# Kernel tuning notes

Measured on AMD Instinct MI355X. Metric: run time of the kernel, lower is better.

Reference implementation:

```python
import jax, jax.numpy as jnp
import numpy as np

N = 100000   # nodes
E = 1600000  # edges (before self-loops)
F_IN = 128
H = 64
G = 512      # graphs in batch


def _add_self_loops(edge_index, n):
    loop = jnp.arange(n, dtype=edge_index.dtype)
    src = jnp.concatenate([edge_index[0], loop])
    dst = jnp.concatenate([edge_index[1], loop])
    return src, dst


def _gcn_norm(src, dst, n):
    # PyG GCNConv: deg over targets with self-loops, norm = d^-1/2[src]*d^-1/2[dst]
    deg = jax.ops.segment_sum(jnp.ones_like(dst, dtype=jnp.float32), dst, num_segments=n)
    dinv = jnp.where(deg > 0, jax.lax.rsqrt(deg), 0.0)
    return dinv[src] * dinv[dst]


def _gcn_conv(x, src, dst, norm, W, b):
    xw = x @ W                                # [N, H]
    msg = xw[src] * norm[:, None]             # [E+N, H] gather + scale
    out = jax.ops.segment_sum(msg, dst, num_segments=x.shape[0])
    return out + b


def setup_inputs() -> dict:
    key = jax.random.key(0)
    ks = jax.random.split(key, 9)
    x = jax.random.normal(ks[0], (N, F_IN), dtype=jnp.float32)
    edge_index = jax.random.randint(ks[1], (2, E), 0, N, dtype=jnp.int32)
    batch = jnp.sort(jax.random.randint(ks[2], (N,), 0, G, dtype=jnp.int32))
    s1 = 1.0 / np.sqrt(F_IN)
    s2 = 1.0 / np.sqrt(H)
    W1 = jax.random.uniform(ks[3], (F_IN, H), jnp.float32, -s1, s1)
    b1 = jnp.zeros((H,), jnp.float32)
    W2 = jax.random.uniform(ks[4], (H, H), jnp.float32, -s2, s2)
    b2 = jnp.zeros((H,), jnp.float32)
    Wl = jax.random.uniform(ks[5], (H, 1), jnp.float32, -s2, s2)
    bl = jnp.zeros((1,), jnp.float32)
    return {"x": x, "edge_index": edge_index, "batch": batch,
            "W1": W1, "b1": b1, "W2": W2, "b2": b2, "Wl": Wl, "bl": bl}


def reference(x, edge_index, batch, W1, b1, W2, b2, Wl, bl):
    n = x.shape[0]
    src, dst = _add_self_loops(edge_index, n)
    norm = _gcn_norm(src, dst, n)
    h = jax.nn.relu(_gcn_conv(x, src, dst, norm, W1, b1))
    h = jax.nn.relu(_gcn_conv(h, src, dst, norm, W2, b2))
    # global mean pool over graphs
    sums = jax.ops.segment_sum(h, batch, num_segments=G)          # [G, H]
    cnt = jax.ops.segment_sum(jnp.ones((n,), jnp.float32), batch, num_segments=G)
    pooled = sums / jnp.maximum(cnt, 1.0)[:, None]
    return jax.nn.sigmoid(pooled @ Wl + bl)                        # [G, 1]
```

## Files before the change

### kernel.cpp

```cpp
#include <hip/hip_runtime.h>
#include <hip/hip_bf16.h>
#include <cmath>

#define F_IN 128
#define HDIM 64
#define NPB 128
#define NB1 512
#define CAP 2560

typedef __attribute__((ext_vector_type(8))) short bf16x8;
typedef __attribute__((ext_vector_type(4))) float f32x4;
typedef __attribute__((ext_vector_type(2))) float f32x2;

__device__ __forceinline__ float bf2f(unsigned short u) {
    union { unsigned int i; float f; } v; v.i = ((unsigned int)u) << 16; return v.f;
}
__device__ __forceinline__ unsigned short f2bf(float f) {
    __hip_bfloat16 h = __float2bfloat16(f);
    union { __hip_bfloat16 h; unsigned short u; } c; c.h = h; return c.u;
}
__device__ __forceinline__ unsigned char f2fp8(float f) {
    int p = __builtin_amdgcn_cvt_pk_fp8_f32(f, f, 0, false);
    return (unsigned char)(p & 0xff);
}
__device__ __forceinline__ void fp8x8_acc(uint2 v, float* a) {
    f32x2 f;
    f = __builtin_amdgcn_cvt_pk_f32_fp8(v.x, false); a[0] += f.x; a[1] += f.y;
    f = __builtin_amdgcn_cvt_pk_f32_fp8(v.x, true);  a[2] += f.x; a[3] += f.y;
    f = __builtin_amdgcn_cvt_pk_f32_fp8(v.y, false); a[4] += f.x; a[5] += f.y;
    f = __builtin_amdgcn_cvt_pk_f32_fp8(v.y, true);  a[6] += f.x; a[7] += f.y;
}


__launch_bounds__(256)
__global__ void p0_count(const int* __restrict__ dst, int* __restrict__ blk_cnt,
                         int E, int nbuk, int chunk,
                         const float* __restrict__ W1, const float* __restrict__ W2,
                         unsigned short* __restrict__ w1t, unsigned short* __restrict__ w2t) {
    int tid = threadIdx.x;
    if (blockIdx.x >= NB1) {
        int t = (blockIdx.x - NB1) * 256 + tid;
        if (t < F_IN * 64) {
            int c = t & 63, k = t >> 6;
            w1t[c * F_IN + k] = f2bf(W1[t]);
        } else if (t < F_IN * 64 + HDIM * 64) {
            int u = t - F_IN * 64;
            int c = u & 63, k = u >> 6;
            w2t[c * HDIM + k] = f2bf(W2[u]);
        }
        return;
    }
    __shared__ int hist[1024];
    for (int i = tid; i < nbuk; i += 256) hist[i] = 0;
    __syncthreads();
    int lo = blockIdx.x * chunk, hi = min(E, lo + chunk);
    for (int e = lo + tid; e < hi; e += 256)
        atomicAdd(&hist[dst[e] >> 7], 1);
    __syncthreads();
    for (int i = tid; i < nbuk; i += 256)
        blk_cnt[(size_t)i * NB1 + blockIdx.x] = hist[i];
}


__launch_bounds__(256)
__global__ void p_scan_blocks(int* __restrict__ blk_cnt, int* __restrict__ bucket_cnt,
                              int nbuk, const int* __restrict__ batch,
                              int* __restrict__ gstart, int n, int G) {
    int tid = threadIdx.x;
    if (blockIdx.x >= nbuk) {
        int g = (blockIdx.x - nbuk) * 256 + tid;
        if (g > G) return;
        int lo = 0, hi = n;
        while (lo < hi) {
            int mid = (lo + hi) >> 1;
            if (batch[mid] < g) lo = mid + 1; else hi = mid;
        }
        gstart[g] = lo;
        return;
    }
    __shared__ int sd[256];
    int b = blockIdx.x;
    int2* row = (int2*)(blk_cnt + (size_t)b * NB1);
    int2 v = row[tid];
    int s0 = v.x, s1 = s0 + v.y;
    sd[tid] = s1;
    __syncthreads();
    for (int off = 1; off < 256; off <<= 1) {
        int a = (tid >= off) ? sd[tid - off] : 0;
        __syncthreads();
        sd[tid] += a;
        __syncthreads();
    }
    int base = sd[tid] - s1;
    row[tid] = make_int2(base, base + s0);
    if (tid == 255) bucket_cnt[b] = sd[255];
}


__launch_bounds__(256)
__global__ void p1_place(const int* __restrict__ src, const int* __restrict__ dst,
                         const int* __restrict__ blk_cnt, int* __restrict__ pairs,
                         int E, int nbuk, int chunk) {
    __shared__ int cur[1024];
    int tid = threadIdx.x;
    for (int i = tid; i < nbuk; i += 256)
        cur[i] = i * CAP + blk_cnt[(size_t)i * NB1 + blockIdx.x];
    __syncthreads();
    int lo = blockIdx.x * chunk, hi = min(E, lo + chunk);
    for (int e = lo + tid; e < hi; e += 256) {
        int d = dst[e];
        int pos = atomicAdd(&cur[d >> 7], 1);
        pairs[pos] = (src[e] << 7) | (d & 127);
    }
}


__launch_bounds__(256)
__global__ void p2_csr(const int* __restrict__ pairs, const int* __restrict__ bucket_cnt,
                       float* __restrict__ dinv, int* __restrict__ col,
                       int4* __restrict__ slot_hdr, int n) {
    __shared__ int dl[128];
    __shared__ int sc[128];
    __shared__ int cur[128];
    __shared__ int h64[64];
    __shared__ int s64[64];
    int b = blockIdx.x, tid = threadIdx.x;
    int nlo = b << 7;
    int eb = b * CAP;
    int ee = eb + bucket_cnt[b];
    if (tid < 128) dl[tid] = 0;
    if (tid < 64) h64[tid] = 0;
    __syncthreads();
    for (int e = eb + tid; e < ee; e += 256)
        atomicAdd(&dl[pairs[e] & 127], 1);
    __syncthreads();
    int d0 = 0, excl = 0;
    if (tid < 128) { d0 = dl[tid]; sc[tid] = d0; }
    __syncthreads();
    for (int off = 1; off < 128; off <<= 1) {
        int a = (tid >= off && tid < 128) ? sc[tid - off] : 0;
        __syncthreads();
        if (tid < 128) sc[tid] += a;
        __syncthreads();
    }
    if (tid < 128) {
        excl = sc[tid] - d0;
        int node = nlo + tid;
        float dv = rsqrtf((float)(d0 + 1));
        if (node < n) dinv[node] = dv;
        cur[tid] = eb + excl;
        atomicAdd(&h64[min(d0, 63)], 1);
    }
    __syncthreads();
    if (tid == 0) { int run = 0; for (int i = 0; i < 64; ++i) { s64[i] = run; run += h64[i]; } }
    __syncthreads();
    if (tid < 64) h64[tid] = 0;
    __syncthreads();
    if (tid < 128) {
        int node = nlo + tid;
        int bin = min(d0, 63);
        int pos = s64[bin] + atomicAdd(&h64[bin], 1);
        int4 hdr;
        hdr.x = (node < n) ? node : 0x7fffffff;
        hdr.y = eb + excl;
        hdr.z = d0;
        hdr.w = __float_as_int(rsqrtf((float)(d0 + 1)));
        slot_hdr[nlo + pos] = hdr;
    }
    __syncthreads();
    for (int e = eb + tid; e < ee; e += 256) {
        unsigned int v = (unsigned int)pairs[e];
        int pos = atomicAdd(&cur[v & 127], 1);
        col[pos] = (int)(v >> 7);
    }
}


template <int K>
__launch_bounds__(256)
__global__ void matmul_mfma(const float* __restrict__ X, const unsigned short* __restrict__ Wt,
                            const float* __restrict__ dinv, unsigned char* __restrict__ out,
                            int n) {
    constexpr int KS  = K / 32;
    constexpr int LDX = K + 8;
    __shared__ unsigned short Xs[64 * LDX];
    __shared__ unsigned short Ws[64 * LDX];
    int tid = threadIdx.x;
    int rowbase = blockIdx.x * 64;
    for (int i = tid; i < 64 * (K / 8); i += 256) {
        int r = i / (K / 8), ch = i % (K / 8);
        *(bf16x8*)(Ws + r * LDX + ch * 8) = ((const bf16x8*)Wt)[i];
    }
    {
        const float4* X4 = (const float4*)X;
        for (int i = tid; i < 64 * (K / 4); i += 256) {
            int r = i / (K / 4), k4 = i % (K / 4);
            ushort4 u = { 0, 0, 0, 0 };
            int gr = rowbase + r;
            if (gr < n) {
                float4 v = X4[(size_t)gr * (K / 4) + k4];
                u.x = f2bf(v.x); u.y = f2bf(v.y); u.z = f2bf(v.z); u.w = f2bf(v.w);
            }
            *(ushort4*)(Xs + r * LDX + k4 * 4) = u;
        }
    }
    __syncthreads();
    int wave = tid >> 6, lane = tid & 63;
    int q = lane >> 4, nn = lane & 15;
    f32x4 acc[4] = {{0,0,0,0},{0,0,0,0},{0,0,0,0},{0,0,0,0}};
    int mrow = wave * 16 + nn;
#pragma unroll
    for (int s = 0; s < KS; ++s) {
        bf16x8 af = *(const bf16x8*)(Xs + mrow * LDX + s * 32 + q * 8);
#pragma unroll
        for (int c = 0; c < 4; ++c) {
            bf16x8 bf = *(const bf16x8*)(Ws + (c * 16 + nn) * LDX + s * 32 + q * 8);
            acc[c] = __builtin_amdgcn_mfma_f32_16x16x32_bf16(af, bf, acc[c], 0, 0, 0);
        }
    }
#pragma unroll
    for (int r = 0; r < 4; ++r) {
        int row = rowbase + wave * 16 + q * 4 + r;
        if (row >= n) continue;
        float dv = dinv[row];
#pragma unroll
        for (int c = 0; c < 4; ++c)
            out[(size_t)row * HDIM + c * 16 + nn] = f2fp8(acc[c][r] * dv);
    }
}


__launch_bounds__(256)
__global__ void gather1_mm2(const int4* __restrict__ slot_hdr, const int* __restrict__ col,
                            const uint2* __restrict__ xws, const float* __restrict__ bias,
                            const unsigned short* __restrict__ w2t,
                            unsigned char* __restrict__ out8, int nslots, int n) {
    __shared__ unsigned short Hs[32 * 72];
    __shared__ unsigned short Ws[64 * 72];
    __shared__ int   snode[32];
    __shared__ float sdinv[32];

    int tid = threadIdx.x;
    int ls = tid >> 3;
    int L  = tid & 7;
    int slot = blockIdx.x * 32 + ls;

    for (int i = tid; i < 64 * 8; i += 256) {
        int r = i >> 3, ch = i & 7;
        *(bf16x8*)(Ws + r * 72 + ch * 8) = ((const bf16x8*)w2t)[i];
    }

    int node = 0x7fffffff;
    float dv = 0.0f;
    float a[8] = {0, 0, 0, 0, 0, 0, 0, 0};
    if (slot < nslots) {
        int4 hdr = slot_hdr[slot];
        node = hdr.x;
        if (node < n) {
            int s = hdr.y, end = s + hdr.z;
            dv = __int_as_float(hdr.w);
            fp8x8_acc(xws[(size_t)node * 8 + L], a);
            int e = s;
            for (; e + 8 <= end; e += 8) {
                uint2 v0 = xws[(size_t)col[e + 0] * 8 + L];
                uint2 v1 = xws[(size_t)col[e + 1] * 8 + L];
                uint2 v2 = xws[(size_t)col[e + 2] * 8 + L];
                uint2 v3 = xws[(size_t)col[e + 3] * 8 + L];
                uint2 v4 = xws[(size_t)col[e + 4] * 8 + L];
                uint2 v5 = xws[(size_t)col[e + 5] * 8 + L];
                uint2 v6 = xws[(size_t)col[e + 6] * 8 + L];
                uint2 v7 = xws[(size_t)col[e + 7] * 8 + L];
                fp8x8_acc(v0, a); fp8x8_acc(v1, a); fp8x8_acc(v2, a); fp8x8_acc(v3, a);
                fp8x8_acc(v4, a); fp8x8_acc(v5, a); fp8x8_acc(v6, a); fp8x8_acc(v7, a);
            }
            for (; e < end; ++e)
                fp8x8_acc(xws[(size_t)col[e] * 8 + L], a);
        }
    }
    if (L == 0) { snode[ls] = node; sdinv[ls] = dv; }
    {
        int f0 = L * 8;
        bf16x8 o;
        if (node < n) {
#pragma unroll
            for (int j = 0; j < 8; ++j)
                o[j] = (short)f2bf(fmaxf(fmaf(a[j], dv, bias[f0 + j]), 0.0f));
        } else {
            short z[8] = {0,0,0,0,0,0,0,0};
            o = *(bf16x8*)z;
        }
        *(bf16x8*)(Hs + ls * 72 + L * 8) = o;
    }
    __syncthreads();

    int wave = tid >> 6, lane = tid & 63;
    int q = lane >> 4, nn = lane & 15;
    int mt  = wave & 1;
    int nt0 = (wave >> 1) * 2;
    f32x4 acc[2] = {{0,0,0,0},{0,0,0,0}};
#pragma unroll
    for (int s = 0; s < 2; ++s) {
        bf16x8 af = *(const bf16x8*)(Hs + (mt * 16 + nn) * 72 + s * 32 + q * 8);
#pragma unroll
        for (int t = 0; t < 2; ++t) {
            bf16x8 bf = *(const bf16x8*)(Ws + ((nt0 + t) * 16 + nn) * 72 + s * 32 + q * 8);
            acc[t] = __builtin_amdgcn_mfma_f32_16x16x32_bf16(af, bf, acc[t], 0, 0, 0);
        }
    }
#pragma unroll
    for (int r = 0; r < 4; ++r) {
        int lslot = mt * 16 + q * 4 + r;
        int nd = snode[lslot];
        if (nd >= n) continue;
        float dvr = sdinv[lslot];
#pragma unroll
        for (int t = 0; t < 2; ++t)
            out8[(size_t)nd * HDIM + (nt0 + t) * 16 + nn] = f2fp8(acc[t][r] * dvr);
    }
}


__launch_bounds__(256)
__global__ void csr_gather8_fp8(const int4* __restrict__ slot_hdr, const int* __restrict__ col,
                                const uint2* __restrict__ xws, const float* __restrict__ bias,
                                bf16x8* __restrict__ outb, int nslots, int n) {
    int t = blockIdx.x * 256 + threadIdx.x;
    int slot = t >> 3;
    if (slot >= nslots) return;
    int L = t & 7;
    int4 hdr = slot_hdr[slot];
    int node = hdr.x;
    if (node >= n) return;
    int s = hdr.y, end = s + hdr.z;
    float dv = __int_as_float(hdr.w);

    float a[8] = {0, 0, 0, 0, 0, 0, 0, 0};
    fp8x8_acc(xws[(size_t)node * 8 + L], a);
    int e = s;
    for (; e + 8 <= end; e += 8) {
        uint2 v0 = xws[(size_t)col[e + 0] * 8 + L];
        uint2 v1 = xws[(size_t)col[e + 1] * 8 + L];
        uint2 v2 = xws[(size_t)col[e + 2] * 8 + L];
        uint2 v3 = xws[(size_t)col[e + 3] * 8 + L];
        uint2 v4 = xws[(size_t)col[e + 4] * 8 + L];
        uint2 v5 = xws[(size_t)col[e + 5] * 8 + L];
        uint2 v6 = xws[(size_t)col[e + 6] * 8 + L];
        uint2 v7 = xws[(size_t)col[e + 7] * 8 + L];
        fp8x8_acc(v0, a); fp8x8_acc(v1, a); fp8x8_acc(v2, a); fp8x8_acc(v3, a);
        fp8x8_acc(v4, a); fp8x8_acc(v5, a); fp8x8_acc(v6, a); fp8x8_acc(v7, a);
    }
    for (; e < end; ++e)
        fp8x8_acc(xws[(size_t)col[e] * 8 + L], a);

    int f0 = L * 8;
    bf16x8 o;
#pragma unroll
    for (int j = 0; j < 8; ++j)
        o[j] = (short)f2bf(fmaxf(fmaf(a[j], dv, bias[f0 + j]), 0.0f));
    outb[(size_t)node * 8 + L] = o;
}


__launch_bounds__(256)
__global__ void pool_head(const unsigned short* __restrict__ h, const int* __restrict__ gstart,
                          const float* __restrict__ Wl, const float* __restrict__ bl,
                          float* __restrict__ out, int G) {
    int g = blockIdx.x;
    int s = gstart[g], e = gstart[g + 1];
    int f  = threadIdx.x & 63;
    int rg = threadIdx.x >> 6;
    float acc = 0.0f;
    for (int i = s + rg; i < e; i += 4)
        acc += bf2f(h[(size_t)i * HDIM + f]);
    __shared__ float red[4][HDIM];
    red[rg][f] = acc;
    __syncthreads();
    if (rg == 0) {
        float v = (red[0][f] + red[1][f]) + (red[2][f] + red[3][f]);
        float c = fmaxf((float)(e - s), 1.0f);
        v = v * Wl[f] * (1.0f / c);
#pragma unroll
        for (int off = 32; off; off >>= 1) v += __shfl_down(v, off, 64);
        if (f == 0) out[g] = 1.0f / (1.0f + expf(-(v + bl[0])));
    }
}


extern "C" void kernel_launch(void* const* d_in, const int* in_sizes, int n_in,
                              void* d_out, int out_size, void* d_ws, size_t ws_size,
                              hipStream_t stream) {
    const float* x   = (const float*)d_in[0];
    const int* ei    = (const int*)d_in[1];
    const int* batch = (const int*)d_in[2];
    const float* W1  = (const float*)d_in[3];
    const float* b1  = (const float*)d_in[4];
    const float* W2  = (const float*)d_in[5];
    const float* b2  = (const float*)d_in[6];
    const float* Wl  = (const float*)d_in[7];
    const float* bl  = (const float*)d_in[8];
    float* out = (float*)d_out;

    const int n = in_sizes[0] / F_IN;
    const int E = in_sizes[1] / 2;
    const int G = out_size;

    const int* srcp = ei;
    const int* dstp = ei + E;

    int nbuk = (n + NPB - 1) / NPB;
    int nslots = nbuk * NPB;

    char* wsb = (char*)d_ws;
    auto alloc = [&](size_t bytes) { char* p = wsb; wsb += (bytes + 255) & ~(size_t)255; return p; };
    float* dinv       = (float*)alloc((size_t)n * 4);
    int4*  slot_hdr   = (int4*)alloc((size_t)nslots * 16);
    int*   bucket_cnt = (int*)alloc(1024 * 4);
    int*   blk_cnt    = (int*)alloc((size_t)nbuk * NB1 * 4);
    int*   pairs      = (int*)alloc((size_t)nbuk * CAP * 4);
    int*   colx       = (int*)alloc((size_t)nbuk * CAP * 4);
    unsigned short* w1t  = (unsigned short*)alloc((size_t)F_IN * HDIM * 2);
    unsigned short* w2t  = (unsigned short*)alloc((size_t)HDIM * HDIM * 2);
    unsigned char*  xws8 = (unsigned char*)alloc((size_t)n * HDIM);
    unsigned char*  xws8b= (unsigned char*)alloc((size_t)n * HDIM);
    unsigned short* xh2  = (unsigned short*)alloc((size_t)n * HDIM * 2);
    int*   gstart     = (int*)alloc(((size_t)G + 1) * 4);

    const int TB = 256;
    int gMM  = (n + 63) / 64;
    int chunk = (E + NB1 - 1) / NB1;
    int gG8  = (nslots * 8 + TB - 1) / TB;
    int gS   = (nslots + 31) / 32;

    p0_count<<<NB1 + 48, TB, 0, stream>>>(dstp, blk_cnt, E, nbuk, chunk, W1, W2, w1t, w2t);
    p_scan_blocks<<<nbuk + 3, TB, 0, stream>>>(blk_cnt, bucket_cnt, nbuk, batch, gstart, n, G);
    p1_place<<<NB1, TB, 0, stream>>>(srcp, dstp, blk_cnt, pairs, E, nbuk, chunk);
    p2_csr<<<nbuk, TB, 0, stream>>>(pairs, bucket_cnt, dinv, colx, slot_hdr, n);

    matmul_mfma<F_IN><<<gMM, TB, 0, stream>>>(x, w1t, dinv, xws8, n);
    gather1_mm2<<<gS, TB, 0, stream>>>(slot_hdr, colx, (const uint2*)xws8,
                                       b1, w2t, xws8b, nslots, n);
    csr_gather8_fp8<<<gG8, TB, 0, stream>>>(slot_hdr, colx, (const uint2*)xws8b,
                                            b2, (bf16x8*)xh2, nslots, n);
    pool_head<<<G, TB, 0, stream>>>(xh2, gstart, Wl, bl, out, G);
}
```

Measured before the change: 238.8 us.

## Merge bucket counting into placement, fuse layer-2 gather with pooling, prefetch col indices

Result: slower. 262.2 us (+9.8%).

```diff
diff --git a/kernel.cpp b/kernel.cpp
--- a/kernel.cpp
+++ b/kernel.cpp
@@ -12,9 +12,6 @@
 typedef __attribute__((ext_vector_type(4))) float f32x4;
 typedef __attribute__((ext_vector_type(2))) float f32x2;
 
-__device__ __forceinline__ float bf2f(unsigned short u) {
-    union { unsigned int i; float f; } v; v.i = ((unsigned int)u) << 16; return v.f;
-}
 __device__ __forceinline__ unsigned short f2bf(float f) {
     __hip_bfloat16 h = __float2bfloat16(f);
     union { __hip_bfloat16 h; unsigned short u; } c; c.h = h; return c.u;
@@ -31,45 +28,62 @@
     f = __builtin_amdgcn_cvt_pk_f32_fp8(v.y, true);  a[6] += f.x; a[7] += f.y;
 }
 
-
-__launch_bounds__(256)
-__global__ void p0_count(const int* __restrict__ dst, int* __restrict__ blk_cnt,
-                         int E, int nbuk, int chunk,
-                         const float* __restrict__ W1, const float* __restrict__ W2,
-                         unsigned short* __restrict__ w1t, unsigned short* __restrict__ w2t) {
-    int tid = threadIdx.x;
-    if (blockIdx.x >= NB1) {
-        int t = (blockIdx.x - NB1) * 256 + tid;
-        if (t < F_IN * 64) {
-            int c = t & 63, k = t >> 6;
-            w1t[c * F_IN + k] = f2bf(W1[t]);
-        } else if (t < F_IN * 64 + HDIM * 64) {
-            int u = t - F_IN * 64;
-            int c = u & 63, k = u >> 6;
-            w2t[c * HDIM + k] = f2bf(W2[u]);
-        }
+__device__ __forceinline__ void gather_rows(const int* __restrict__ col,
+                                            const uint2* __restrict__ xws,
+                                            int L, int s, int end, float* a) {
+    int e = s;
+    int c[8];
+    bool have = (e + 8 <= end);
+    if (have) {
+#pragma unroll
+        for (int i = 0; i < 8; ++i) c[i] = col[e + i];
+    }
+    while (have) {
+        uint2 v0 = xws[(size_t)c[0] * 8 + L];
+        uint2 v1 = xws[(size_t)c[1] * 8 + L];
+        uint2 v2 = xws[(size_t)c[2] * 8 + L];
+        uint2 v3 = xws[(size_t)c[3] * 8 + L];
+        uint2 v4 = xws[(size_t)c[4] * 8 + L];
+        uint2 v5 = xws[(size_t)c[5] * 8 + L];
+        uint2 v6 = xws[(size_t)c[6] * 8 + L];
+        uint2 v7 = xws[(size_t)c[7] * 8 + L];
+        int e2 = e + 8;
+        bool nxt = (e2 + 8 <= end);
+        int d[8];
+#pragma unroll
+        for (int i = 0; i < 8; ++i) d[i] = nxt ? col[e2 + i] : 0;
+        fp8x8_acc(v0, a); fp8x8_acc(v1, a); fp8x8_acc(v2, a); fp8x8_acc(v3, a);
+        fp8x8_acc(v4, a); fp8x8_acc(v5, a); fp8x8_acc(v6, a); fp8x8_acc(v7, a);
+#pragma unroll
+        for (int i = 0; i < 8; ++i) c[i] = d[i];
+        e = e2; have = nxt;
+    }
+    for (; e < end; ++e)
+        fp8x8_acc(xws[(size_t)col[e] * 8 + L], a);
+}
+
+
+__launch_bounds__(256)
+__global__ void k_init(const float* __restrict__ W1, const float* __restrict__ W2,
+                       unsigned short* __restrict__ w1t, unsigned short* __restrict__ w2t,
+                       const int* __restrict__ batch, int* __restrict__ gstart,
+                       int n, int G, int* __restrict__ gcnt, int nbuk,
+                       float* __restrict__ pooled) {
+    int t = blockIdx.x * 256 + threadIdx.x;
+    if (t < F_IN * 64) {
+        int c = t & 63, k = t >> 6;
+        w1t[c * F_IN + k] = f2bf(W1[t]);
         return;
     }
-    __shared__ int hist[1024];
-    for (int i = tid; i < nbuk; i += 256) hist[i] = 0;
-    __syncthreads();
-    int lo = blockIdx.x * chunk, hi = min(E, lo + chunk);
-    for (int e = lo + tid; e < hi; e += 256)
-        atomicAdd(&hist[dst[e] >> 7], 1);
-    __syncthreads();
-    for (int i = tid; i < nbuk; i += 256)
-        blk_cnt[(size_t)i * NB1 + blockIdx.x] = hist[i];
-}
-
-
-__launch_bounds__(256)
-__global__ void p_scan_blocks(int* __restrict__ blk_cnt, int* __restrict__ bucket_cnt,
-                              int nbuk, const int* __restrict__ batch,
-                              int* __restrict__ gstart, int n, int G) {
-    int tid = threadIdx.x;
-    if (blockIdx.x >= nbuk) {
-        int g = (blockIdx.x - nbuk) * 256 + tid;
-        if (g > G) return;
+    t -= F_IN * 64;
+    if (t < HDIM * 64) {
+        int c = t & 63, k = t >> 6;
+        w2t[c * HDIM + k] = f2bf(W2[t]);
+        return;
+    }
+    t -= HDIM * 64;
+    if (t <= G) {
+        int g = t;
         int lo = 0, hi = n;
         while (lo < hi) {
             int mid = (lo + hi) >> 1;
@@ -78,35 +92,31 @@
         gstart[g] = lo;
         return;
     }
-    __shared__ int sd[256];
-    int b = blockIdx.x;
-    int2* row = (int2*)(blk_cnt + (size_t)b * NB1);
-    int2 v = row[tid];
-    int s0 = v.x, s1 = s0 + v.y;
-    sd[tid] = s1;
-    __syncthreads();
-    for (int off = 1; off < 256; off <<= 1) {
-        int a = (tid >= off) ? sd[tid - off] : 0;
-        __syncthreads();
-        sd[tid] += a;
-        __syncthreads();
-    }
-    int base = sd[tid] - s1;
-    row[tid] = make_int2(base, base + s0);
-    if (tid == 255) bucket_cnt[b] = sd[255];
-}
-
-
-__launch_bounds__(256)
-__global__ void p1_place(const int* __restrict__ src, const int* __restrict__ dst,
-                         const int* __restrict__ blk_cnt, int* __restrict__ pairs,
-                         int E, int nbuk, int chunk) {
+    t -= G + 1;
+    if (t < nbuk) { gcnt[t] = 0; return; }
+    t -= nbuk;
+    if (t < G * HDIM) pooled[t] = 0.0f;
+}
+
+
+__launch_bounds__(256)
+__global__ void p_place(const int* __restrict__ src, const int* __restrict__ dst,
+                        int* __restrict__ gcnt, int* __restrict__ pairs,
+                        int E, int nbuk, int chunk) {
+    __shared__ int hist[1024];
     __shared__ int cur[1024];
     int tid = threadIdx.x;
-    for (int i = tid; i < nbuk; i += 256)
-        cur[i] = i * CAP + blk_cnt[(size_t)i * NB1 + blockIdx.x];
+    for (int i = tid; i < nbuk; i += 256) hist[i] = 0;
     __syncthreads();
     int lo = blockIdx.x * chunk, hi = min(E, lo + chunk);
+    for (int e = lo + tid; e < hi; e += 256)
+        atomicAdd(&hist[dst[e] >> 7], 1);
+    __syncthreads();
+    for (int i = tid; i < nbuk; i += 256) {
+        int c = hist[i];
+        cur[i] = i * CAP + (c ? atomicAdd(&gcnt[i], c) : 0);
+    }
+    __syncthreads();
     for (int e = lo + tid; e < hi; e += 256) {
         int d = dst[e];
         int pos = atomicAdd(&cur[d >> 7], 1);
@@ -119,6 +129,7 @@
 __global__ void p2_csr(const int* __restrict__ pairs, const int* __restrict__ bucket_cnt,
                        float* __restrict__ dinv, int* __restrict__ col,
                        int4* __restrict__ slot_hdr, int n) {
+    __shared__ int plds[CAP];
     __shared__ int dl[128];
     __shared__ int sc[128];
     __shared__ int cur[128];
@@ -127,12 +138,15 @@
     int b = blockIdx.x, tid = threadIdx.x;
     int nlo = b << 7;
     int eb = b * CAP;
-    int ee = eb + bucket_cnt[b];
+    int cnt = bucket_cnt[b];
     if (tid < 128) dl[tid] = 0;
     if (tid < 64) h64[tid] = 0;
     __syncthreads();
-    for (int e = eb + tid; e < ee; e += 256)
-        atomicAdd(&dl[pairs[e] & 127], 1);
+    for (int i = tid; i < cnt; i += 256) {
+        int v = pairs[eb + i];
+        plds[i] = v;
+        atomicAdd(&dl[v & 127], 1);
+    }
     __syncthreads();
     int d0 = 0, excl = 0;
     if (tid < 128) { d0 = dl[tid]; sc[tid] = d0; }
@@ -168,8 +182,8 @@
         slot_hdr[nlo + pos] = hdr;
     }
     __syncthreads();
-    for (int e = eb + tid; e < ee; e += 256) {
-        unsigned int v = (unsigned int)pairs[e];
+    for (int i = tid; i < cnt; i += 256) {
+        unsigned int v = (unsigned int)plds[i];
         int pos = atomicAdd(&cur[v & 127], 1);
         col[pos] = (int)(v >> 7);
     }
@@ -260,21 +274,7 @@
             int s = hdr.y, end = s + hdr.z;
             dv = __int_as_float(hdr.w);
             fp8x8_acc(xws[(size_t)node * 8 + L], a);
-            int e = s;
-            for (; e + 8 <= end; e += 8) {
-                uint2 v0 = xws[(size_t)col[e + 0] * 8 + L];
-                uint2 v1 = xws[(size_t)col[e + 1] * 8 + L];
-                uint2 v2 = xws[(size_t)col[e + 2] * 8 + L];
-                uint2 v3 = xws[(size_t)col[e + 3] * 8 + L];
-                uint2 v4 = xws[(size_t)col[e + 4] * 8 + L];
-                uint2 v5 = xws[(size_t)col[e + 5] * 8 + L];
-                uint2 v6 = xws[(size_t)col[e + 6] * 8 + L];
-                uint2 v7 = xws[(size_t)col[e + 7] * 8 + L];
-                fp8x8_acc(v0, a); fp8x8_acc(v1, a); fp8x8_acc(v2, a); fp8x8_acc(v3, a);
-                fp8x8_acc(v4, a); fp8x8_acc(v5, a); fp8x8_acc(v6, a); fp8x8_acc(v7, a);
-            }
-            for (; e < end; ++e)
-                fp8x8_acc(xws[(size_t)col[e] * 8 + L], a);
+            gather_rows(col, xws, L, s, end, a);
         }
     }
     if (L == 0) { snode[ls] = node; sdinv[ls] = dv; }
@@ -321,68 +321,82 @@
 
 
 __launch_bounds__(256)
-__global__ void csr_gather8_fp8(const int4* __restrict__ slot_hdr, const int* __restrict__ col,
-                                const uint2* __restrict__ xws, const float* __restrict__ bias,
-                                bf16x8* __restrict__ outb, int nslots, int n) {
-    int t = blockIdx.x * 256 + threadIdx.x;
-    int slot = t >> 3;
-    if (slot >= nslots) return;
-    int L = t & 7;
-    int4 hdr = slot_hdr[slot];
-    int node = hdr.x;
-    if (node >= n) return;
-    int s = hdr.y, end = s + hdr.z;
-    float dv = __int_as_float(hdr.w);
+__global__ void gather2_pool(const int4* __restrict__ slot_hdr, const int* __restrict__ col,
+                             const uint2* __restrict__ xws, const float* __restrict__ bias,
+                             const int* __restrict__ batch, float* __restrict__ pooled,
+                             int nslots, int n, int G) {
+    __shared__ float lpool[4][HDIM];
+    __shared__ int sg[32];
+    __shared__ int sgmin;
+    int tid = threadIdx.x;
+    int ls = tid >> 3;
+    int L  = tid & 7;
+    int slot = blockIdx.x * 32 + ls;
+
+    lpool[tid >> 6][tid & 63] = 0.0f;
+    if (tid == 0) sgmin = 0x7fffffff;
+
+    int node = 0x7fffffff;
+    float dv = 0.0f;
+    int s = 0, deg = 0;
+    if (slot < nslots) {
+        int4 hdr = slot_hdr[slot];
+        node = hdr.x;
+        if (node < n) { s = hdr.y; deg = hdr.z; dv = __int_as_float(hdr.w); }
+    }
+    if (L == 0) {
+        int g = (node < n) ? batch[node] : 0x7fffffff;
+        sg[ls] = g;
+        if (node < n) atomicMin(&sgmin, g);
+    }
 
     float a[8] = {0, 0, 0, 0, 0, 0, 0, 0};
-    fp8x8_acc(xws[(size_t)node * 8 + L], a);
-    int e = s;
-    for (; e + 8 <= end; e += 8) {
-        uint2 v0 = xws[(size_t)col[e + 0] * 8 + L];
-        uint2 v1 = xws[(size_t)col[e + 1] * 8 + L];
-        uint2 v2 = xws[(size_t)col[e + 2] * 8 + L];
-        uint2 v3 = xws[(size_t)col[e + 3] * 8 + L];
-        uint2 v4 = xws[(size_t)col[e + 4] * 8 + L];
-        uint2 v5 = xws[(size_t)col[e + 5] * 8 + L];
-        uint2 v6 = xws[(size_t)col[e + 6] * 8 + L];
-        uint2 v7 = xws[(size_t)col[e + 7] * 8 + L];
-        fp8x8_acc(v0, a); fp8x8_acc(v1, a); fp8x8_acc(v2, a); fp8x8_acc(v3, a);
-        fp8x8_acc(v4, a); fp8x8_acc(v5, a); fp8x8_acc(v6, a); fp8x8_acc(v7, a);
-    }
-    for (; e < end; ++e)
-        fp8x8_acc(xws[(size_t)col[e] * 8 + L], a);
-
-    int f0 = L * 8;
-    bf16x8 o;
-#pragma unroll
-    for (int j = 0; j < 8; ++j)
-        o[j] = (short)f2bf(fmaxf(fmaf(a[j], dv, bias[f0 + j]), 0.0f));
-    outb[(size_t)node * 8 + L] = o;
-}
-
-
-__launch_bounds__(256)
-__global__ void pool_head(const unsigned short* __restrict__ h, const int* __restrict__ gstart,
-                          const float* __restrict__ Wl, const float* __restrict__ bl,
-                          float* __restrict__ out, int G) {
-    int g = blockIdx.x;
-    int s = gstart[g], e = gstart[g + 1];
-    int f  = threadIdx.x & 63;
-    int rg = threadIdx.x >> 6;
-    float acc = 0.0f;
-    for (int i = s + rg; i < e; i += 4)
-        acc += bf2f(h[(size_t)i * HDIM + f]);
-    __shared__ float red[4][HDIM];
-    red[rg][f] = acc;
-    __syncthreads();
-    if (rg == 0) {
-        float v = (red[0][f] + red[1][f]) + (red[2][f] + red[3][f]);
-        float c = fmaxf((float)(e - s), 1.0f);
-        v = v * Wl[f] * (1.0f / c);
-#pragma unroll
-        for (int off = 32; off; off >>= 1) v += __shfl_down(v, off, 64);
-        if (f == 0) out[g] = 1.0f / (1.0f + expf(-(v + bl[0])));
-    }
+    if (node < n) {
+        fp8x8_acc(xws[(size_t)node * 8 + L], a);
+        gather_rows(col, xws, L, s, s + deg, a);
+    }
+    __syncthreads();
+
+    int gmin = sgmin;
+    if (node < n) {
+        int g  = sg[ls];
+        int gl = g - gmin;
+        int f0 = L * 8;
+        if (gl < 4) {
+#pragma unroll
+            for (int j = 0; j < 8; ++j)
+                atomicAdd(&lpool[gl][f0 + j], fmaxf(fmaf(a[j], dv, bias[f0 + j]), 0.0f));
+        } else {
+#pragma unroll
+            for (int j = 0; j < 8; ++j)
+                atomicAdd(&pooled[(size_t)g * HDIM + f0 + j],
+                          fmaxf(fmaf(a[j], dv, bias[f0 + j]), 0.0f));
+        }
+    }
+    __syncthreads();
+
+    if (gmin != 0x7fffffff) {
+        int r = tid >> 6, f = tid & 63;
+        float v = lpool[r][f];
+        int gg = gmin + r;
+        if (v != 0.0f && gg < G)
+            atomicAdd(&pooled[(size_t)gg * HDIM + f], v);
+    }
+}
+
+
+__launch_bounds__(256)
+__global__ void head(const float* __restrict__ pooled, const int* __restrict__ gstart,
+                     const float* __restrict__ Wl, const float* __restrict__ bl,
+                     float* __restrict__ out, int G) {
+    int g = blockIdx.x * 4 + (threadIdx.x >> 6);
+    int f = threadIdx.x & 63;
+    if (g >= G) return;
+    float cnt = fmaxf((float)(gstart[g + 1] - gstart[g]), 1.0f);
+    float v = pooled[(size_t)g * HDIM + f] * Wl[f] * (1.0f / cnt);
+#pragma unroll
+    for (int off = 32; off; off >>= 1) v += __shfl_down(v, off, 64);
+    if (f == 0) out[g] = 1.0f / (1.0f + expf(-(v + bl[0])));
 }
 
 
@@ -414,32 +428,31 @@
     auto alloc = [&](size_t bytes) { char* p = wsb; wsb += (bytes + 255) & ~(size_t)255; return p; };
     float* dinv       = (float*)alloc((size_t)n * 4);
     int4*  slot_hdr   = (int4*)alloc((size_t)nslots * 16);
-    int*   bucket_cnt = (int*)alloc(1024 * 4);
-    int*   blk_cnt    = (int*)alloc((size_t)nbuk * NB1 * 4);
+    int*   gcnt       = (int*)alloc(1024 * 4);
     int*   pairs      = (int*)alloc((size_t)nbuk * CAP * 4);
     int*   colx       = (int*)alloc((size_t)nbuk * CAP * 4);
     unsigned short* w1t  = (unsigned short*)alloc((size_t)F_IN * HDIM * 2);
     unsigned short* w2t  = (unsigned short*)alloc((size_t)HDIM * HDIM * 2);
     unsigned char*  xws8 = (unsigned char*)alloc((size_t)n * HDIM);
     unsigned char*  xws8b= (unsigned char*)alloc((size_t)n * HDIM);
-    unsigned short* xh2  = (unsigned short*)alloc((size_t)n * HDIM * 2);
+    float* pooled     = (float*)alloc((size_t)G * HDIM * 4);
     int*   gstart     = (int*)alloc(((size_t)G + 1) * 4);
 
     const int TB = 256;
     int gMM  = (n + 63) / 64;
     int chunk = (E + NB1 - 1) / NB1;
-    int gG8  = (nslots * 8 + TB - 1) / TB;
     int gS   = (nslots + 31) / 32;
-
-    p0_count<<<NB1 + 48, TB, 0, stream>>>(dstp, blk_cnt, E, nbuk, chunk, W1, W2, w1t, w2t);
-    p_scan_blocks<<<nbuk + 3, TB, 0, stream>>>(blk_cnt, bucket_cnt, nbuk, batch, gstart, n, G);
-    p1_place<<<NB1, TB, 0, stream>>>(srcp, dstp, blk_cnt, pairs, E, nbuk, chunk);
-    p2_csr<<<nbuk, TB, 0, stream>>>(pairs, bucket_cnt, dinv, colx, slot_hdr, n);
-
+    int initWork = F_IN * 64 + HDIM * 64 + (G + 1) + nbuk + G * HDIM;
+    int gInit = (initWork + TB - 1) / TB;
+
+    k_init<<<gInit, TB, 0, stream>>>(W1, W2, w1t, w2t, batch, gstart, n, G,
+                                     gcnt, nbuk, pooled);
+    p_place<<<NB1, TB, 0, stream>>>(srcp, dstp, gcnt, pairs, E, nbuk, chunk);
+    p2_csr<<<nbuk, TB, 0, stream>>>(pairs, gcnt, dinv, colx, slot_hdr, n);
     matmul_mfma<F_IN><<<gMM, TB, 0, stream>>>(x, w1t, dinv, xws8, n);
     gather1_mm2<<<gS, TB, 0, stream>>>(slot_hdr, colx, (const uint2*)xws8,
                                        b1, w2t, xws8b, nslots, n);
-    csr_gather8_fp8<<<gG8, TB, 0, stream>>>(slot_hdr, colx, (const uint2*)xws8b,
-                                            b2, (bf16x8*)xh2, nslots, n);
-    pool_head<<<G, TB, 0, stream>>>(xh2, gstart, Wl, bl, out, G);
-}
+    gather2_pool<<<gS, TB, 0, stream>>>(slot_hdr, colx, (const uint2*)xws8b,
+                                        b2, batch, pooled, nslots, n, G);
+    head<<<(G + 3) / 4, TB, 0, stream>>>(pooled, gstart, Wl, bl, out, G);
+}
```
